# Optimization experiments

Hardware: AMD Instinct MI355X
Metric: run time of the kernel (lower is better)

## Reference

```python
import jax, jax.numpy as jnp
import numpy as np

B, S, H = 8, 2048, 2048

def setup_inputs() -> dict:
    key = jax.random.key(0)
    ks = jax.random.split(key, 7)
    return {
        "time_decay": jax.random.normal(ks[0], (H,), dtype=jnp.float32),
        "key": jax.random.normal(ks[1], (B, S, H), dtype=jnp.float32),
        "time_first": jax.random.normal(ks[2], (H,), dtype=jnp.float32),
        "value": jax.random.normal(ks[3], (B, S, H), dtype=jnp.float32),
        "max_state": jax.random.normal(ks[4], (B, H), dtype=jnp.float32),
        "num_state": jax.random.normal(ks[5], (B, H), dtype=jnp.float32),
        "den_state": jax.random.uniform(ks[6], (B, H), dtype=jnp.float32),
    }

def _wkv(time_decay, k, time_first, v, max_state, num_state, den_state):
    f32 = jnp.float32
    td = -jnp.exp(time_decay.astype(f32))          # [H]
    tf = time_first.astype(f32)                    # [H]
    k = k.astype(f32)
    v = v.astype(f32)

    def step(carry, kv_t):
        m, num, den = carry                        # each [B,H]
        kt, vt = kv_t                              # each [B,H]
        # output branch: include time_first bonus
        mo = jnp.maximum(m, kt + tf)
        e1o = jnp.exp(m - mo)
        e2o = jnp.exp(kt + tf - mo)
        out = (e1o * num + e2o * vt) / (e1o * den + e2o)
        # state branch: apply decay
        ms = jnp.maximum(m + td, kt)
        e1s = jnp.exp(m + td - ms)
        e2s = jnp.exp(kt - ms)
        return (ms, e1s * num + e2s * vt, e1s * den + e2s), out

    carry0 = (max_state.astype(f32), num_state.astype(f32), den_state.astype(f32))
    # scan over time: move seq axis to front -> [S,B,H]
    (m, num, den), outs = jax.lax.scan(
        step, carry0, (jnp.swapaxes(k, 0, 1), jnp.swapaxes(v, 0, 1)))
    output = jnp.swapaxes(outs, 0, 1)              # [B,S,H]
    return output, m, num, den

def reference(time_decay, key, time_first, value, max_state, num_state, den_state):
    return _wkv(time_decay, key, time_first, value, max_state, num_state, den_state)
```

## Files before the change

kernel.cpp:

```cpp
#include <hip/hip_runtime.h>


#define TILE   128
#define NW     8
#define WSTEPS 16
#define SUBL   8

#define BARR  asm volatile("s_waitcnt lgkmcnt(0)\n\ts_barrier" ::: "memory")

__device__ __forceinline__ float ex2(float x)  { return __builtin_amdgcn_exp2f(x); }
__device__ __forceinline__ float rcpf(float x) { return __builtin_amdgcn_rcpf(x); }

__device__ __forceinline__ void merge(float& M, float& N, float& D,
                                      float dlen, float sm, float sn, float sd)
{
    const float Md = M + dlen;
    const float d  = Md - sm;
    const float e  = ex2(-fabsf(d));
    const bool  c  = d >= 0.f;
    const float a  = c ? 1.f : e;
    const float bb = c ? e : 1.f;
    N = a * N + bb * sn;
    D = a * D + bb * sd;
    M = fmaxf(Md, sm);
}

__global__ __launch_bounds__(512, 4)
void wkv_fwd(const float* __restrict__ td_in, const float* __restrict__ kin,
             const float* __restrict__ tf_in, const float* __restrict__ vin,
             const float* __restrict__ m0, const float* __restrict__ n0,
             const float* __restrict__ d0,
             float* __restrict__ out, float* __restrict__ m_out,
             float* __restrict__ n_out, float* __restrict__ dn_out,
             int B, int S, int H)
{
    __shared__ float smry[2][NW][3][32];
    __shared__ float cry[2][3][32];

    const int tid  = threadIdx.x;
    const int lane = tid & 63;
    const int w    = tid >> 6;
    const int c    = lane & 31;
    const int s    = lane >> 5;

    const int bpb = H >> 5;
    const int b   = blockIdx.x / bpb;
    const int hb  = (blockIdx.x - b * bpb) << 5;
    const int h   = hb + c;
    const int g   = b * H + h;

    constexpr float Cc = 1.4426950408889634f;
    constexpr float IC = 0.6931471805599453f;

    const float tds    = -ex2(td_in[h] * Cc) * Cc;
    const float tfs    = tf_in[h] * Cc;
    const float dseg8  = tds * (float)SUBL;
    const float dseg16 = tds * (float)WSTEPS;

    if (w == 0 && s == 0) {
        cry[0][0][c] = m0[g] * Cc;
        cry[0][1][c] = n0[g];
        cry[0][2][c] = d0[g];
    }

    const size_t base = (size_t)b * (size_t)S * (size_t)H + (size_t)hb;
    const float* gk = kin + base;
    const float* gv = vin + base;
    float*       go = out + base;

    const int row0   = w * WSTEPS + s * SUBL;
    const int ntiles = S / TILE;

    float fM = 0.f, fN = 0.f, fD = 0.f;

    float ka[SUBL], va[SUBL], kb[SUBL], vb[SUBL];

    #pragma unroll
    for (int j = 0; j < SUBL; ++j) {
        ka[j] = gk[(size_t)(row0 + j) * (size_t)H + c];
        va[j] = gv[(size_t)(row0 + j) * (size_t)H + c];
    }

    auto body = [&](int it, float (&ck)[SUBL], float (&cv)[SUBL],
                    float (&nk)[SUBL], float (&nv)[SUBL])
                __attribute__((always_inline)) -> void {
        if (it + 1 < ntiles) {
            const size_t r1 = (size_t)(it + 1) * TILE + row0;
            #pragma unroll
            for (int j = 0; j < SUBL; ++j) {
                nk[j] = gk[(r1 + j) * (size_t)H + c];
                nv[j] = gv[(r1 + j) * (size_t)H + c];
            }
        }

        const int p = it & 1;

        float lm = -1e30f, ln = 0.f, ld = 0.f;
        #pragma unroll
        for (int j = 0; j < SUBL; ++j) {
            const float kt = ck[j] * Cc;
            ck[j] = kt;
            const float vt  = cv[j];
            const float mpd = lm + tds;
            const float d   = mpd - kt;
            const float e   = ex2(-fabsf(d));
            const bool  cc  = d >= 0.f;
            const float e1  = cc ? 1.f : e;
            const float e2  = cc ? e : 1.f;
            ln = e1 * ln + e2 * vt;
            ld = e1 * ld + e2;
            lm = fmaxf(mpd, kt);
        }

        const float om = __shfl_xor(lm, 32);
        const float on = __shfl_xor(ln, 32);
        const float od = __shfl_xor(ld, 32);

        float wm = s ? om : lm, wn = s ? on : ln, wd = s ? od : ld;
        {
            const float sm2 = s ? lm : om;
            const float sn2 = s ? ln : on;
            const float sd2 = s ? ld : od;
            merge(wm, wn, wd, dseg8, sm2, sn2, sd2);
        }
        if (s == 0) {
            smry[p][w][0][c] = wm;
            smry[p][w][1][c] = wn;
            smry[p][w][2][c] = wd;
        }
        BARR;

        float M = cry[p][0][c];
        float N = cry[p][1][c];
        float D = cry[p][2][c];
        #pragma unroll
        for (int j = 0; j < NW - 1; ++j) {
            const float sm = smry[p][j][0][c];
            const float sn = smry[p][j][1][c];
            const float sd = smry[p][j][2][c];
            if (j < w) merge(M, N, D, dseg16, sm, sn, sd);
        }

        if (w == NW - 1 && s == 0) {
            fM = M; fN = N; fD = D;
            merge(fM, fN, fD, dseg16, wm, wn, wd);
            cry[p ^ 1][0][c] = fM;
            cry[p ^ 1][1][c] = fN;
            cry[p ^ 1][2][c] = fD;
        }

        if (s == 1) merge(M, N, D, dseg8, om, on, od);

        float* po = go + ((size_t)it * TILE + row0) * (size_t)H;
        #pragma unroll
        for (int j = 0; j < SUBL; ++j) {
            const float kt  = ck[j];
            const float vt  = cv[j];
            const float ktf = kt + tfs;
            const float dd  = M - ktf;
            const float eo  = ex2(-fabsf(dd));
            const bool  co  = dd >= 0.f;
            const float e1o = co ? 1.f : eo;
            const float e2o = co ? eo : 1.f;
            po[(size_t)j * H + c] =
                (e1o * N + e2o * vt) * rcpf(fmaf(e1o, D, e2o));
            const float mpd = M + tds;
            const float ds_ = mpd - kt;
            const float es  = ex2(-fabsf(ds_));
            const bool  cs  = ds_ >= 0.f;
            const float e1s = cs ? 1.f : es;
            const float e2s = cs ? es : 1.f;
            N = e1s * N + e2s * vt;
            D = e1s * D + e2s;
            M = fmaxf(mpd, kt);
        }
    };

    int it = 0;
    for (; it + 1 < ntiles; it += 2) {
        body(it,     ka, va, kb, vb);
        body(it + 1, kb, vb, ka, va);
    }
    if (it < ntiles) body(it, ka, va, kb, vb);

    if (w == NW - 1 && s == 0) {
        m_out[g]  = fM * IC;
        n_out[g]  = fN;
        dn_out[g] = fD;
    }
}

__global__ __launch_bounds__(64)
void wkv_fwd_serial(const float* __restrict__ td_in, const float* __restrict__ kin,
                    const float* __restrict__ tf_in, const float* __restrict__ vin,
                    const float* __restrict__ m0, const float* __restrict__ n0,
                    const float* __restrict__ d0,
                    float* __restrict__ out, float* __restrict__ m_out,
                    float* __restrict__ n_out, float* __restrict__ dn_out,
                    int B, int S, int H)
{
    const int g = blockIdx.x * 64 + threadIdx.x;
    if (g >= B * H) return;
    const int b = g / H;
    const int h = g - b * H;
    constexpr float Cc = 1.4426950408889634f, IC = 0.6931471805599453f;
    const float tds = -ex2(td_in[h] * Cc) * Cc;
    const float tfs = tf_in[h] * Cc;
    float M = m0[g] * Cc, N = n0[g], D = d0[g];
    const size_t base = (size_t)b * S * H + h;
    for (int t = 0; t < S; ++t) {
        const float kt  = kin[base + (size_t)t * H] * Cc;
        const float vt  = vin[base + (size_t)t * H];
        const float ktf = kt + tfs;
        const float mo  = fmaxf(M, ktf);
        const float e1o = ex2(M - mo), e2o = ex2(ktf - mo);
        out[base + (size_t)t * H] = (e1o * N + e2o * vt) * rcpf(e1o * D + e2o);
        const float mpd = M + tds;
        const float ms  = fmaxf(mpd, kt);
        const float e1s = ex2(mpd - ms), e2s = ex2(kt - ms);
        N = e1s * N + e2s * vt;
        D = e1s * D + e2s;
        M = ms;
    }
    m_out[g] = M * IC; n_out[g] = N; dn_out[g] = D;
}

extern "C" void kernel_launch(void* const* d_in, const int* in_sizes, int n_in,
                              void* d_out, int out_size, void* d_ws, size_t ws_size,
                              hipStream_t stream)
{
    const float* time_decay = (const float*)d_in[0];
    const float* key        = (const float*)d_in[1];
    const float* time_first = (const float*)d_in[2];
    const float* value      = (const float*)d_in[3];
    const float* max_state  = (const float*)d_in[4];
    const float* num_state  = (const float*)d_in[5];
    const float* den_state  = (const float*)d_in[6];

    const int H  = in_sizes[0];
    const int BH = in_sizes[4];
    const int B  = BH / H;
    const int S  = in_sizes[1] / BH;

    float* out    = (float*)d_out;
    float* m_out  = out + (size_t)B * (size_t)S * (size_t)H;
    float* n_out  = m_out + BH;
    float* dn_out = n_out + BH;

    if ((H % 32 == 0) && (S % TILE == 0)) {
        const int grid = BH / 32;
        wkv_fwd<<<grid, 512, 0, stream>>>(time_decay, key, time_first, value,
                                          max_state, num_state, den_state,
                                          out, m_out, n_out, dn_out, B, S, H);
    } else {
        const int grid = (BH + 63) / 64;
        wkv_fwd_serial<<<grid, 64, 0, stream>>>(time_decay, key, time_first, value,
                                                max_state, num_state, den_state,
                                                out, m_out, n_out, dn_out, B, S, H);
    }
}
```

Before: 350.5 us.

## Add single-pass decoupled look-back scan kernel over sequence chunks

Adds a new kernel that splits each batch/channel-group chain into 8-step sequence chunks, one block per chunk, with each thread handling four channels through vectorized nontemporal loads and stores. Each block computes a local chunk summary, publishes it through global flags, and looks back over its predecessors' aggregate or inclusive prefixes to get its carry-in. If a flag is not set after a bounded spin, it recomputes that predecessor's summary from the raw k and v. The aim is to expose far more parallelism along the sequence than the per-block serial tile loop, so the work runs closer to memory bandwidth. The cost is a large workspace for prefix planes, extra global traffic, a flag memset, and reliance on blocks being scheduled roughly in order.

```diff
diff --git a/kernel.cpp b/kernel.cpp
--- a/kernel.cpp
+++ b/kernel.cpp
@@ -1,18 +1,19 @@
 #include <hip/hip_runtime.h>
 
 
-#define TILE   128
-#define NW     8
-#define WSTEPS 16
-#define SUBL   8
-
-#define BARR  asm volatile("s_waitcnt lgkmcnt(0)\n\ts_barrier" ::: "memory")
+#define LCH   8
+#define CPB   4
+#define THR   256
+#define GCH   1024
+#define SPINM 65536
+
+typedef float f4v __attribute__((ext_vector_type(4)));
 
 __device__ __forceinline__ float ex2(float x)  { return __builtin_amdgcn_exp2f(x); }
 __device__ __forceinline__ float rcpf(float x) { return __builtin_amdgcn_rcpf(x); }
 
-__device__ __forceinline__ void merge(float& M, float& N, float& D,
-                                      float dlen, float sm, float sn, float sd)
+__device__ __forceinline__ void merge1(float& M, float& N, float& D,
+                                       float dlen, float sm, float sn, float sd)
 {
     const float Md = M + dlen;
     const float d  = Md - sm;
@@ -25,16 +26,253 @@
     M = fmaxf(Md, sm);
 }
 
+__global__ __launch_bounds__(THR, 4)
+void wkv_fwd_lb(const float* __restrict__ td_in, const float* __restrict__ kin,
+                const float* __restrict__ tf_in, const float* __restrict__ vin,
+                const float* __restrict__ m0, const float* __restrict__ n0,
+                const float* __restrict__ d0,
+                float* __restrict__ out, float* __restrict__ m_out,
+                float* __restrict__ n_out, float* __restrict__ dn_out,
+                int* __restrict__ flags,
+                float* __restrict__ agm, float* __restrict__ agn, float* __restrict__ agd,
+                float* __restrict__ icm, float* __restrict__ icn, float* __restrict__ icd,
+                int B, int S, int H, int nchain, int NC)
+{
+    __shared__ int shf;
+    const int tid   = threadIdx.x;
+    const int bid   = blockIdx.x;
+    const int chain = bid % nchain;
+    const int i     = bid / nchain;
+    const int hgpb  = H / GCH;
+    const int b     = chain / hgpb;
+    const int hg    = chain - b * hgpb;
+    const int ch    = hg * GCH + tid * CPB;
+    const int g0    = b * H + ch;
+
+    constexpr float Cc = 1.4426950408889634f;
+    constexpr float IC = 0.6931471805599453f;
+
+    float tds[CPB], tfs[CPB];
+    {
+        const f4v t4 = *reinterpret_cast<const f4v*>(td_in + ch);
+        const f4v f4 = *reinterpret_cast<const f4v*>(tf_in + ch);
+        #pragma unroll
+        for (int c = 0; c < CPB; ++c) {
+            tds[c] = -ex2(t4[c] * Cc) * Cc;
+            tfs[c] = f4[c] * Cc;
+        }
+    }
+
+    const size_t rowbase = ((size_t)b * S + (size_t)i * LCH) * H + ch;
+    f4v kq[LCH], vq[LCH];
+    #pragma unroll
+    for (int j = 0; j < LCH; ++j) {
+        kq[j] = __builtin_nontemporal_load(
+                    reinterpret_cast<const f4v*>(kin + rowbase + (size_t)j * H));
+        vq[j] = __builtin_nontemporal_load(
+                    reinterpret_cast<const f4v*>(vin + rowbase + (size_t)j * H));
+    }
+
+    float lm[CPB], ln[CPB], ld[CPB];
+    #pragma unroll
+    for (int c = 0; c < CPB; ++c) { lm[c] = -1e30f; ln[c] = 0.f; ld[c] = 0.f; }
+    #pragma unroll
+    for (int j = 0; j < LCH; ++j) {
+        #pragma unroll
+        for (int c = 0; c < CPB; ++c) {
+            const float kt  = kq[j][c] * Cc;
+            const float vt  = vq[j][c];
+            const float mpd = lm[c] + tds[c];
+            const float d   = mpd - kt;
+            const float e   = ex2(-fabsf(d));
+            const bool  cc  = d >= 0.f;
+            const float e1  = cc ? 1.f : e;
+            const float e2  = cc ? e : 1.f;
+            ln[c] = e1 * ln[c] + e2 * vt;
+            ld[c] = e1 * ld[c] + e2;
+            lm[c] = fmaxf(mpd, kt);
+        }
+    }
+
+    const size_t myoff = (size_t)bid * GCH + (size_t)tid * CPB;
+
+    if (i > 0 && i < NC - 1) {
+        #pragma unroll
+        for (int c = 0; c < CPB; ++c) {
+            __hip_atomic_store(agm + myoff + c, lm[c], __ATOMIC_RELAXED, __HIP_MEMORY_SCOPE_AGENT);
+            __hip_atomic_store(agn + myoff + c, ln[c], __ATOMIC_RELAXED, __HIP_MEMORY_SCOPE_AGENT);
+            __hip_atomic_store(agd + myoff + c, ld[c], __ATOMIC_RELAXED, __HIP_MEMORY_SCOPE_AGENT);
+        }
+        __syncthreads();
+        if (tid == 0)
+            __hip_atomic_store(flags + bid, 1, __ATOMIC_RELEASE, __HIP_MEMORY_SCOPE_AGENT);
+    }
+
+    float bM[CPB], bN[CPB], bD[CPB];
+    if (i == 0) {
+        const f4v a4 = *reinterpret_cast<const f4v*>(m0 + g0);
+        const f4v b4 = *reinterpret_cast<const f4v*>(n0 + g0);
+        const f4v c4 = *reinterpret_cast<const f4v*>(d0 + g0);
+        #pragma unroll
+        for (int c = 0; c < CPB; ++c) {
+            bM[c] = a4[c] * Cc; bN[c] = b4[c]; bD[c] = c4[c];
+        }
+    } else {
+        #pragma unroll
+        for (int c = 0; c < CPB; ++c) { bM[c] = -1e30f; bN[c] = 0.f; bD[c] = 0.f; }
+        int cnt = 0, pred = i - 1;
+        bool done = false;
+        while (!done) {
+            if (tid == 0) {
+                int ff, t = 0;
+                do {
+                    ff = __hip_atomic_load(flags + ((size_t)pred * nchain + chain),
+                                           __ATOMIC_ACQUIRE, __HIP_MEMORY_SCOPE_AGENT);
+                } while (ff == 0 && ++t < SPINM);
+                shf = ff;
+            }
+            __syncthreads();
+            const int f2 = shf;
+            __syncthreads();
+            const size_t poff = ((size_t)pred * nchain + chain) * GCH + (size_t)tid * CPB;
+            float am[CPB], an[CPB], ad[CPB];
+            if (f2 == 2) {
+                #pragma unroll
+                for (int c = 0; c < CPB; ++c) {
+                    am[c] = __hip_atomic_load(icm + poff + c, __ATOMIC_RELAXED, __HIP_MEMORY_SCOPE_AGENT);
+                    an[c] = __hip_atomic_load(icn + poff + c, __ATOMIC_RELAXED, __HIP_MEMORY_SCOPE_AGENT);
+                    ad[c] = __hip_atomic_load(icd + poff + c, __ATOMIC_RELAXED, __HIP_MEMORY_SCOPE_AGENT);
+                    merge1(am[c], an[c], ad[c], tds[c] * (float)(LCH * cnt), bM[c], bN[c], bD[c]);
+                    bM[c] = am[c]; bN[c] = an[c]; bD[c] = ad[c];
+                }
+                done = true;
+            } else {
+                if (f2 == 1) {
+                    #pragma unroll
+                    for (int c = 0; c < CPB; ++c) {
+                        am[c] = __hip_atomic_load(agm + poff + c, __ATOMIC_RELAXED, __HIP_MEMORY_SCOPE_AGENT);
+                        an[c] = __hip_atomic_load(agn + poff + c, __ATOMIC_RELAXED, __HIP_MEMORY_SCOPE_AGENT);
+                        ad[c] = __hip_atomic_load(agd + poff + c, __ATOMIC_RELAXED, __HIP_MEMORY_SCOPE_AGENT);
+                    }
+                } else {
+                    #pragma unroll
+                    for (int c = 0; c < CPB; ++c) { am[c] = -1e30f; an[c] = 0.f; ad[c] = 0.f; }
+                    const size_t pb = ((size_t)b * S + (size_t)pred * LCH) * H + ch;
+                    for (int j = 0; j < LCH; ++j) {
+                        const f4v kk = *reinterpret_cast<const f4v*>(kin + pb + (size_t)j * H);
+                        const f4v vv = *reinterpret_cast<const f4v*>(vin + pb + (size_t)j * H);
+                        #pragma unroll
+                        for (int c = 0; c < CPB; ++c) {
+                            const float kt  = kk[c] * Cc;
+                            const float vt  = vv[c];
+                            const float mpd = am[c] + tds[c];
+                            const float d   = mpd - kt;
+                            const float e   = ex2(-fabsf(d));
+                            const bool  cc  = d >= 0.f;
+                            const float e1  = cc ? 1.f : e;
+                            const float e2  = cc ? e : 1.f;
+                            an[c] = e1 * an[c] + e2 * vt;
+                            ad[c] = e1 * ad[c] + e2;
+                            am[c] = fmaxf(mpd, kt);
+                        }
+                    }
+                }
+                #pragma unroll
+                for (int c = 0; c < CPB; ++c) {
+                    merge1(am[c], an[c], ad[c], tds[c] * (float)(LCH * cnt), bM[c], bN[c], bD[c]);
+                    bM[c] = am[c]; bN[c] = an[c]; bD[c] = ad[c];
+                }
+                ++cnt; --pred;
+                if (pred < 0) {
+                    const f4v a4 = *reinterpret_cast<const f4v*>(m0 + g0);
+                    const f4v b4 = *reinterpret_cast<const f4v*>(n0 + g0);
+                    const f4v c4 = *reinterpret_cast<const f4v*>(d0 + g0);
+                    #pragma unroll
+                    for (int c = 0; c < CPB; ++c) {
+                        am[c] = a4[c] * Cc; an[c] = b4[c]; ad[c] = c4[c];
+                        merge1(am[c], an[c], ad[c], tds[c] * (float)(LCH * cnt), bM[c], bN[c], bD[c]);
+                        bM[c] = am[c]; bN[c] = an[c]; bD[c] = ad[c];
+                    }
+                    done = true;
+                }
+            }
+        }
+    }
+
+    {
+        float iM[CPB], iN[CPB], iD[CPB];
+        #pragma unroll
+        for (int c = 0; c < CPB; ++c) {
+            iM[c] = bM[c]; iN[c] = bN[c]; iD[c] = bD[c];
+            merge1(iM[c], iN[c], iD[c], tds[c] * (float)LCH, lm[c], ln[c], ld[c]);
+        }
+        if (i < NC - 1) {
+            #pragma unroll
+            for (int c = 0; c < CPB; ++c) {
+                __hip_atomic_store(icm + myoff + c, iM[c], __ATOMIC_RELAXED, __HIP_MEMORY_SCOPE_AGENT);
+                __hip_atomic_store(icn + myoff + c, iN[c], __ATOMIC_RELAXED, __HIP_MEMORY_SCOPE_AGENT);
+                __hip_atomic_store(icd + myoff + c, iD[c], __ATOMIC_RELAXED, __HIP_MEMORY_SCOPE_AGENT);
+            }
+            __syncthreads();
+            if (tid == 0)
+                __hip_atomic_store(flags + bid, 2, __ATOMIC_RELEASE, __HIP_MEMORY_SCOPE_AGENT);
+        } else {
+            f4v a4, b4, c4;
+            #pragma unroll
+            for (int c = 0; c < CPB; ++c) {
+                a4[c] = iM[c] * IC; b4[c] = iN[c]; c4[c] = iD[c];
+            }
+            *reinterpret_cast<f4v*>(m_out  + g0) = a4;
+            *reinterpret_cast<f4v*>(n_out  + g0) = b4;
+            *reinterpret_cast<f4v*>(dn_out + g0) = c4;
+        }
+    }
+
+    #pragma unroll
+    for (int j = 0; j < LCH; ++j) {
+        f4v o4;
+        #pragma unroll
+        for (int c = 0; c < CPB; ++c) {
+            const float kt  = kq[j][c] * Cc;
+            const float vt  = vq[j][c];
+            const float ktf = kt + tfs[c];
+            const float dd  = bM[c] - ktf;
+            const float eo  = ex2(-fabsf(dd));
+            const bool  co  = dd >= 0.f;
+            const float e1o = co ? 1.f : eo;
+            const float e2o = co ? eo : 1.f;
+            o4[c] = (e1o * bN[c] + e2o * vt) * rcpf(fmaf(e1o, bD[c], e2o));
+            const float mpd = bM[c] + tds[c];
+            const float ds  = mpd - kt;
+            const float es  = ex2(-fabsf(ds));
+            const bool  cs  = ds >= 0.f;
+            const float e1s = cs ? 1.f : es;
+            const float e2s = cs ? es : 1.f;
+            bN[c] = e1s * bN[c] + e2s * vt;
+            bD[c] = e1s * bD[c] + e2s;
+            bM[c] = fmaxf(mpd, kt);
+        }
+        __builtin_nontemporal_store(o4,
+            reinterpret_cast<f4v*>(out + rowbase + (size_t)j * H));
+    }
+}
+
+#define BTILE   128
+#define BNW     8
+#define BWSTEPS 16
+#define BSUBL   8
+#define BARR  asm volatile("s_waitcnt lgkmcnt(0)\n\ts_barrier" ::: "memory")
+
 __global__ __launch_bounds__(512, 4)
-void wkv_fwd(const float* __restrict__ td_in, const float* __restrict__ kin,
-             const float* __restrict__ tf_in, const float* __restrict__ vin,
-             const float* __restrict__ m0, const float* __restrict__ n0,
-             const float* __restrict__ d0,
-             float* __restrict__ out, float* __restrict__ m_out,
-             float* __restrict__ n_out, float* __restrict__ dn_out,
-             int B, int S, int H)
+void wkv_fwd_blocked(const float* __restrict__ td_in, const float* __restrict__ kin,
+                     const float* __restrict__ tf_in, const float* __restrict__ vin,
+                     const float* __restrict__ m0, const float* __restrict__ n0,
+                     const float* __restrict__ d0,
+                     float* __restrict__ out, float* __restrict__ m_out,
+                     float* __restrict__ n_out, float* __restrict__ dn_out,
+                     int B, int S, int H)
 {
-    __shared__ float smry[2][NW][3][32];
+    __shared__ float smry[2][BNW][3][32];
     __shared__ float cry[2][3][32];
 
     const int tid  = threadIdx.x;
@@ -54,8 +292,8 @@
 
     const float tds    = -ex2(td_in[h] * Cc) * Cc;
     const float tfs    = tf_in[h] * Cc;
-    const float dseg8  = tds * (float)SUBL;
-    const float dseg16 = tds * (float)WSTEPS;
+    const float dseg8  = tds * (float)BSUBL;
+    const float dseg16 = tds * (float)BWSTEPS;
 
     if (w == 0 && s == 0) {
         cry[0][0][c] = m0[g] * Cc;
@@ -68,36 +306,33 @@
     const float* gv = vin + base;
     float*       go = out + base;
 
-    const int row0   = w * WSTEPS + s * SUBL;
-    const int ntiles = S / TILE;
+    const int row0   = w * BWSTEPS + s * BSUBL;
+    const int ntiles = S / BTILE;
 
     float fM = 0.f, fN = 0.f, fD = 0.f;
-
-    float ka[SUBL], va[SUBL], kb[SUBL], vb[SUBL];
+    float ka[BSUBL], va[BSUBL], kb[BSUBL], vb[BSUBL];
 
     #pragma unroll
-    for (int j = 0; j < SUBL; ++j) {
+    for (int j = 0; j < BSUBL; ++j) {
         ka[j] = gk[(size_t)(row0 + j) * (size_t)H + c];
         va[j] = gv[(size_t)(row0 + j) * (size_t)H + c];
     }
 
-    auto body = [&](int it, float (&ck)[SUBL], float (&cv)[SUBL],
-                    float (&nk)[SUBL], float (&nv)[SUBL])
+    auto body = [&](int it, float (&ck)[BSUBL], float (&cv)[BSUBL],
+                    float (&nk)[BSUBL], float (&nv)[BSUBL])
                 __attribute__((always_inline)) -> void {
         if (it + 1 < ntiles) {
-            const size_t r1 = (size_t)(it + 1) * TILE + row0;
+            const size_t r1 = (size_t)(it + 1) * BTILE + row0;
             #pragma unroll
-            for (int j = 0; j < SUBL; ++j) {
+            for (int j = 0; j < BSUBL; ++j) {
                 nk[j] = gk[(r1 + j) * (size_t)H + c];
                 nv[j] = gv[(r1 + j) * (size_t)H + c];
             }
         }
-
         const int p = it & 1;
-
         float lm = -1e30f, ln = 0.f, ld = 0.f;
         #pragma unroll
-        for (int j = 0; j < SUBL; ++j) {
+        for (int j = 0; j < BSUBL; ++j) {
             const float kt = ck[j] * Cc;
             ck[j] = kt;
             const float vt  = cv[j];
@@ -111,17 +346,15 @@
             ld = e1 * ld + e2;
             lm = fmaxf(mpd, kt);
         }
-
         const float om = __shfl_xor(lm, 32);
         const float on = __shfl_xor(ln, 32);
         const float od = __shfl_xor(ld, 32);
-
         float wm = s ? om : lm, wn = s ? on : ln, wd = s ? od : ld;
         {
             const float sm2 = s ? lm : om;
             const float sn2 = s ? ln : on;
             const float sd2 = s ? ld : od;
-            merge(wm, wn, wd, dseg8, sm2, sn2, sd2);
+            merge1(wm, wn, wd, dseg8, sm2, sn2, sd2);
         }
         if (s == 0) {
             smry[p][w][0][c] = wm;
@@ -129,31 +362,27 @@
             smry[p][w][2][c] = wd;
         }
         BARR;
-
         float M = cry[p][0][c];
         float N = cry[p][1][c];
         float D = cry[p][2][c];
         #pragma unroll
-        for (int j = 0; j < NW - 1; ++j) {
+        for (int j = 0; j < BNW - 1; ++j) {
             const float sm = smry[p][j][0][c];
             const float sn = smry[p][j][1][c];
             const float sd = smry[p][j][2][c];
-            if (j < w) merge(M, N, D, dseg16, sm, sn, sd);
-        }
-
-        if (w == NW - 1 && s == 0) {
+            if (j < w) merge1(M, N, D, dseg16, sm, sn, sd);
+        }
+        if (w == BNW - 1 && s == 0) {
             fM = M; fN = N; fD = D;
-            merge(fM, fN, fD, dseg16, wm, wn, wd);
+            merge1(fM, fN, fD, dseg16, wm, wn, wd);
             cry[p ^ 1][0][c] = fM;
             cry[p ^ 1][1][c] = fN;
             cry[p ^ 1][2][c] = fD;
         }
-
-        if (s == 1) merge(M, N, D, dseg8, om, on, od);
-
-        float* po = go + ((size_t)it * TILE + row0) * (size_t)H;
-        #pragma unroll
-        for (int j = 0; j < SUBL; ++j) {
+        if (s == 1) merge1(M, N, D, dseg8, om, on, od);
+        float* po = go + ((size_t)it * BTILE + row0) * (size_t)H;
+        #pragma unroll
+        for (int j = 0; j < BSUBL; ++j) {
             const float kt  = ck[j];
             const float vt  = cv[j];
             const float ktf = kt + tfs;
@@ -183,7 +412,7 @@
     }
     if (it < ntiles) body(it, ka, va, kb, vb);
 
-    if (w == NW - 1 && s == 0) {
+    if (w == BNW - 1 && s == 0) {
         m_out[g]  = fM * IC;
         n_out[g]  = fN;
         dn_out[g] = fD;
@@ -247,12 +476,42 @@
     float* n_out  = m_out + BH;
     float* dn_out = n_out + BH;
 
-    if ((H % 32 == 0) && (S % TILE == 0)) {
+    bool launched = false;
+    if ((H % GCH == 0) && (S % LCH == 0) && d_ws != nullptr) {
+        const int    nchain    = B * (H / GCH);
+        const int    NC        = S / LCH;
+        const size_t rec       = (size_t)nchain * NC;
+        const size_t flagBytes = rec * sizeof(int);
+        const size_t flagOff   = (flagBytes + 1023) & ~(size_t)1023;
+        const size_t planeElems= rec * GCH;
+        const size_t need      = flagOff + 6 * planeElems * sizeof(float);
+        if (ws_size >= need) {
+            int*   flags = (int*)d_ws;
+            float* base0 = (float*)((char*)d_ws + flagOff);
+            float* agm = base0;
+            float* agn = agm + planeElems;
+            float* agd = agn + planeElems;
+            float* icm = agd + planeElems;
+            float* icn = icm + planeElems;
+            float* icd = icn + planeElems;
+            (void)hipMemsetAsync(flags, 0, flagBytes, stream);
+            wkv_fwd_lb<<<(int)rec, THR, 0, stream>>>(
+                time_decay, key, time_first, value,
+                max_state, num_state, den_state,
+                out, m_out, n_out, dn_out,
+                flags, agm, agn, agd, icm, icn, icd,
+                B, S, H, nchain, NC);
+            launched = true;
+        }
+    }
+    if (!launched && (H % 32 == 0) && (S % BTILE == 0)) {
         const int grid = BH / 32;
-        wkv_fwd<<<grid, 512, 0, stream>>>(time_decay, key, time_first, value,
-                                          max_state, num_state, den_state,
-                                          out, m_out, n_out, dn_out, B, S, H);
-    } else {
+        wkv_fwd_blocked<<<grid, 512, 0, stream>>>(time_decay, key, time_first, value,
+                                                  max_state, num_state, den_state,
+                                                  out, m_out, n_out, dn_out, B, S, H);
+        launched = true;
+    }
+    if (!launched) {
         const int grid = (BH + 63) / 64;
         wkv_fwd_serial<<<grid, 64, 0, stream>>>(time_decay, key, time_first, value,
                                                 max_state, num_state, den_state,
```

Result: slower. 1.142 ms (+225.9%).
